# Kernel optimization log

Hardware: AMD Instinct MI355X
Metric: run time of the kernel (lower is better)

## Reference

```python
import jax, jax.numpy as jnp
import numpy as np

B, N, DIM = 4, 2048, 1024
HEADS, DIM_HEAD = 16, 64
INNER = HEADS * DIM_HEAD  # 1024
SCALE = DIM_HEAD ** -0.5

def setup_inputs() -> dict:
    key = jax.random.key(0)
    k1, k2, k3 = jax.random.split(key, 3)
    x = jax.random.normal(k1, (B, N, DIM), dtype=jnp.float32)
    w_qkv = jax.random.normal(k2, (DIM, 3 * INNER), dtype=jnp.float32) * (DIM ** -0.5)
    w_out = jax.random.normal(k3, (INNER, DIM), dtype=jnp.float32) * (INNER ** -0.5)
    b_out = jnp.zeros((DIM,), dtype=jnp.float32)
    return {"x": x, "w_qkv": w_qkv, "w_out": w_out, "b_out": b_out}

def reference(x, w_qkv, w_out, b_out):
    b, n, _ = x.shape
    qkv = x @ w_qkv  # [b, n, 3*inner]
    q, k, v = jnp.split(qkv, 3, axis=-1)
    # [b, n, h, d] -> [b, h, n, d]
    reshape = lambda t: t.reshape(b, n, HEADS, DIM_HEAD).transpose(0, 2, 1, 3)
    q, k, v = reshape(q), reshape(k), reshape(v)
    dots = jnp.einsum('bhqd,bhkd->bhqk', q, k) * SCALE
    attn = jax.nn.softmax(dots, axis=-1)
    out = jnp.einsum('bhqk,bhkd->bhqd', attn, v)
    out = out.transpose(0, 2, 1, 3).reshape(b, n, INNER)
    return out @ w_out + b_out
```

## Files before the change

### kernel.cpp

```cpp
#include <hip/hip_runtime.h>

typedef unsigned short u16;
typedef __bf16 bf16_t;
typedef bf16_t bf16x8 __attribute__((ext_vector_type(8)));
typedef float f32x4 __attribute__((ext_vector_type(4)));
typedef float f32x16 __attribute__((ext_vector_type(16)));
typedef u16 u16x8 __attribute__((ext_vector_type(8)));
typedef u16 u16x4 __attribute__((ext_vector_type(4)));
typedef unsigned uint2v __attribute__((ext_vector_type(2)));

#define B_     4
#define N_     2048
#define DIM_   1024
#define HEADS_ 16
#define DH_    64
#define INNER_ 1024
#define QKV3_  3072
#define SCALE_ 0.125f
#define LOG2E_ 1.44269504089f

__device__ __forceinline__ u16 f2bf(float f) {
  union { float f; unsigned u; } v; v.f = f;
  unsigned r = v.u + 0x7FFFu + ((v.u >> 16) & 1u);
  return (u16)(r >> 16);
}
__device__ __forceinline__ u16 bfbits(float f) {
  bf16_t b = (bf16_t)f;
  return __builtin_bit_cast(u16, b);
}
__device__ __forceinline__ unsigned packbf(float lo, float hi) {
  return (unsigned)bfbits(lo) | ((unsigned)bfbits(hi) << 16);
}

#if __has_builtin(__builtin_amdgcn_exp2f)
#define EXP2F(x) __builtin_amdgcn_exp2f(x)
#else
#define EXP2F(x) __expf((x) * 0.69314718056f)
#endif

typedef __attribute__((address_space(1))) const unsigned int ga_u32;
typedef __attribute__((address_space(3))) unsigned int ls_u32;
__device__ __forceinline__ void gload16(const void* g, void* l) {
  __builtin_amdgcn_global_load_lds((ga_u32*)g, (ls_u32*)l, 16, 0, 0);
}

__global__ __launch_bounds__(256) void cvt_f32_bf16(const float* __restrict__ in,
                                                    u16* __restrict__ out, int n8) {
  int i = blockIdx.x * 256 + threadIdx.x;
  if (i < n8) {
    const float4* p = (const float4*)(in + (size_t)i * 8);
    float4 a = p[0], b = p[1];
    u16x8 o;
    o[0] = f2bf(a.x); o[1] = f2bf(a.y); o[2] = f2bf(a.z); o[3] = f2bf(a.w);
    o[4] = f2bf(b.x); o[5] = f2bf(b.y); o[6] = f2bf(b.z); o[7] = f2bf(b.w);
    *(u16x8*)(out + (size_t)i * 8) = o;
  }
}

__global__ __launch_bounds__(256) void transp_w(const float* __restrict__ in,
                                                u16* __restrict__ out, int Kd, int Nd) {
  __shared__ float t[32][33];
  int n0 = blockIdx.x * 32, k0 = blockIdx.y * 32;
  int tx = threadIdx.x & 31, ty = threadIdx.x >> 5;
#pragma unroll
  for (int i = 0; i < 4; i++)
    t[ty + i * 8][tx] = in[(size_t)(k0 + ty + i * 8) * Nd + n0 + tx];
  __syncthreads();
#pragma unroll
  for (int i = 0; i < 4; i++)
    out[(size_t)(n0 + ty + i * 8) * Kd + k0 + tx] = f2bf(t[tx][ty + i * 8]);
}

__global__ __launch_bounds__(512, 2) void gemm_qkv(const u16* __restrict__ A,
                                                   const u16* __restrict__ BT,
                                                   u16* __restrict__ qbuf,
                                                   u16* __restrict__ ktiled,
                                                   u16* __restrict__ vtiled) {
  constexpr int K = DIM_;
  constexpr int KT = K / 64;
  __shared__ alignas(16) u16 ldsA[2][256 * 64];
  __shared__ alignas(16) u16 ldsB[2][256 * 64];
  const int tid = threadIdx.x;
  const int lane = tid & 63, wid = tid >> 6;
  const int l16 = lane & 15, lg = lane >> 4;
  const int wm = wid >> 2, wn = wid & 3;

  int bid = blockIdx.x;
  bid = (bid & 7) * 48 + (bid >> 3);
  const int tm = bid / 12, tn = bid % 12;
  const int m0 = tm << 8, n0 = tn << 8;

  const int srow_in = lane >> 3;
  const int soff = ((lane & 7) ^ srow_in) * 8;

  f32x4 acc[8][4];
#pragma unroll
  for (int i = 0; i < 8; i++)
#pragma unroll
    for (int j = 0; j < 4; j++) acc[i][j] = f32x4{0.f, 0.f, 0.f, 0.f};

#define STG_(kk, buf)                                                              \
  do {                                                                             \
    const int k1_ = (kk) << 6;                                                     \
    char* bA_ = (char*)&ldsA[(buf)][0];                                            \
    char* bB_ = (char*)&ldsB[(buf)][0];                                            \
    _Pragma("unroll")                                                              \
    for (int i_ = 0; i_ < 4; i_++) {                                               \
      const int rb_ = i_ * 64 + wid * 8;                                           \
      gload16(A  + (size_t)(m0 + rb_ + srow_in) * K + k1_ + soff, bA_ + rb_ * 128);\
      gload16(BT + (size_t)(n0 + rb_ + srow_in) * K + k1_ + soff, bB_ + rb_ * 128);\
    }                                                                              \
  } while (0)

  STG_(0, 0);

  for (int kt = 0; kt < KT; kt++) {
    asm volatile("s_waitcnt vmcnt(0)" ::: "memory");
    __builtin_amdgcn_s_barrier();
    if (kt + 1 < KT) STG_(kt + 1, (kt + 1) & 1);

    const char* cA = (const char*)&ldsA[kt & 1][0];
    const char* cB = (const char*)&ldsB[kt & 1][0];

    bf16x8 bf[4][2];
#pragma unroll
    for (int nf = 0; nf < 4; nf++) {
      const int row = wn * 64 + nf * 16 + l16;
      const int rb = row * 128, swz = (row & 7) << 4;
      bf[nf][0] = *(const bf16x8*)(cB + rb + ((lg * 16) ^ swz));
      bf[nf][1] = *(const bf16x8*)(cB + rb + ((64 + lg * 16) ^ swz));
    }
#pragma unroll
    for (int half = 0; half < 2; half++) {
      bf16x8 af[4][2];
#pragma unroll
      for (int m = 0; m < 4; m++) {
        const int row = wm * 128 + (half * 4 + m) * 16 + l16;
        const int rb = row * 128, swz = (row & 7) << 4;
        af[m][0] = *(const bf16x8*)(cA + rb + ((lg * 16) ^ swz));
        af[m][1] = *(const bf16x8*)(cA + rb + ((64 + lg * 16) ^ swz));
      }
      __builtin_amdgcn_s_setprio(1);
#pragma unroll
      for (int m = 0; m < 4; m++)
#pragma unroll
        for (int nf = 0; nf < 4; nf++) {
          f32x4 c = acc[half * 4 + m][nf];
          c = __builtin_amdgcn_mfma_f32_16x16x32_bf16(af[m][0], bf[nf][0], c, 0, 0, 0);
          c = __builtin_amdgcn_mfma_f32_16x16x32_bf16(af[m][1], bf[nf][1], c, 0, 0, 0);
          acc[half * 4 + m][nf] = c;
        }
      __builtin_amdgcn_s_setprio(0);
    }
  }
#undef STG_

  const int seg = n0 >> 10;
#pragma unroll
  for (int mf = 0; mf < 8; mf++) {
#pragma unroll
    for (int nf = 0; nf < 4; nf++) {
      const int row = m0 + wm * 128 + mf * 16 + lg * 4;
      const int col = n0 + wn * 64 + nf * 16 + l16;
      if (seg == 0) {
#pragma unroll
        for (int j = 0; j < 4; j++)
          qbuf[(size_t)(row + j) * INNER_ + col] = f2bf(acc[mf][nf][j]);
      } else if (seg == 1) {
        const int kd = col - 1024;
        const int h = kd >> 6, s = (kd >> 3) & 7, e = kd & 7;
#pragma unroll
        for (int j = 0; j < 4; j++) {
          const int rr = row + j;
          const int b = rr >> 11, n = rr & (N_ - 1);
          ktiled[(((size_t)(b * HEADS_ + h) * 32 + (n >> 6)) << 12) +
                 (s << 9) + ((n & 63) << 3) + e] = f2bf(acc[mf][nf][j]);
        }
      } else {
        const int vd = col - 2048;
        const int h = vd >> 6, d = vd & 63;
#pragma unroll
        for (int j = 0; j < 4; j++) {
          const int rr = row + j;
          const int b = rr >> 11, n = rr & (N_ - 1);
          vtiled[(((size_t)(b * HEADS_ + h) * 32 + (n >> 6)) << 12) +
                 (((n >> 3) & 7) << 9) + (d << 3) + (n & 7)] = f2bf(acc[mf][nf][j]);
        }
      }
    }
  }
}

__global__ __launch_bounds__(256) void gemm_bt(const u16* __restrict__ A,
                                               const u16* __restrict__ BT,
                                               float* __restrict__ Cp,
                                               const float* __restrict__ bias,
                                               int M, int N, int K) {
  __shared__ alignas(16) u16 ldsA[2][128 * 64];
  __shared__ alignas(16) u16 ldsB[2][128 * 64];
  const int tid = threadIdx.x;
  const int lane = tid & 63, wid = tid >> 6;
  const int l16 = lane & 15, lg = lane >> 4;

  int bid = blockIdx.x;
  const int cpx = gridDim.x >> 3;
  bid = (bid & 7) * cpx + (bid >> 3);

  const int ntiles = N >> 7;
  const int tm = bid / ntiles, tn = bid % ntiles;
  const int m0 = tm << 7, n0 = tn << 7;
  const int wr = wid >> 1, wc = wid & 1;

  const int srow_in = lane >> 3;
  const int soff = ((lane & 7) ^ srow_in) * 8;

  f32x4 acc[4][4];
#pragma unroll
  for (int i = 0; i < 4; i++)
#pragma unroll
    for (int j = 0; j < 4; j++) acc[i][j] = f32x4{0.f, 0.f, 0.f, 0.f};

  const int KSTEPS = K >> 6;

#define GSTAGE_(kk, buf)                                                           \
  do {                                                                             \
    const int k1_ = (kk) << 6;                                                     \
    char* bA_ = (char*)&ldsA[(buf)][0];                                            \
    char* bB_ = (char*)&ldsB[(buf)][0];                                            \
    _Pragma("unroll")                                                              \
    for (int i_ = 0; i_ < 4; i_++) {                                               \
      const int rb_ = wid * 32 + i_ * 8;                                           \
      gload16(A  + (size_t)(m0 + rb_ + srow_in) * K + k1_ + soff, bA_ + rb_ * 128);\
      gload16(BT + (size_t)(n0 + rb_ + srow_in) * K + k1_ + soff, bB_ + rb_ * 128);\
    }                                                                              \
  } while (0)

  GSTAGE_(0, 0);
  GSTAGE_(1, 1);

  for (int ks = 0; ks < KSTEPS; ks++) {
    if (ks + 1 < KSTEPS) asm volatile("s_waitcnt vmcnt(8)" ::: "memory");
    else                 asm volatile("s_waitcnt vmcnt(0)" ::: "memory");
    __builtin_amdgcn_s_barrier();

    const char* cA = (const char*)&ldsA[ks & 1][0];
    const char* cB = (const char*)&ldsB[ks & 1][0];

    bf16x8 bf[4][2];
#pragma unroll
    for (int n = 0; n < 4; n++) {
      int row = wc * 64 + n * 16 + l16;
      int rb = row * 128, swz = (row & 7) << 4;
      bf[n][0] = *(const bf16x8*)(cB + rb + ((lg * 16) ^ swz));
      bf[n][1] = *(const bf16x8*)(cB + rb + ((64 + lg * 16) ^ swz));
    }
    __builtin_amdgcn_s_setprio(1);
#pragma unroll
    for (int mm = 0; mm < 4; mm++) {
      int row = wr * 64 + mm * 16 + l16;
      int rb = row * 128, swz = (row & 7) << 4;
      bf16x8 af0 = *(const bf16x8*)(cA + rb + ((lg * 16) ^ swz));
      bf16x8 af1 = *(const bf16x8*)(cA + rb + ((64 + lg * 16) ^ swz));
#pragma unroll
      for (int n = 0; n < 4; n++) {
        acc[mm][n] = __builtin_amdgcn_mfma_f32_16x16x32_bf16(af0, bf[n][0], acc[mm][n], 0, 0, 0);
        acc[mm][n] = __builtin_amdgcn_mfma_f32_16x16x32_bf16(af1, bf[n][1], acc[mm][n], 0, 0, 0);
      }
    }
    __builtin_amdgcn_s_setprio(0);

    __builtin_amdgcn_s_barrier();
    if (ks + 2 < KSTEPS) GSTAGE_(ks + 2, ks & 1);
  }
#undef GSTAGE_

#pragma unroll
  for (int mm = 0; mm < 4; mm++) {
#pragma unroll
    for (int n = 0; n < 4; n++) {
      int row = m0 + wr * 64 + mm * 16 + lg * 4;
      int col = n0 + wc * 64 + n * 16 + l16;
#pragma unroll
      for (int j = 0; j < 4; j++)
        Cp[(size_t)(row + j) * N + col] = acc[mm][n][j] + bias[col];
    }
  }
}

__global__ __launch_bounds__(512, 4) void attn_fwd(const u16* __restrict__ qbuf,
                                                   const u16* __restrict__ ktiled,
                                                   const u16* __restrict__ vtiled,
                                                   u16* __restrict__ abuf) {
  __shared__ alignas(16) u16 ldsK[3][64 * 64];
  __shared__ alignas(16) u16 ldsV[3][64 * 64];

  const int tid = threadIdx.x;
  const int lane = tid & 63, wid = tid >> 6;
  const int l32 = lane & 31, hl = lane >> 5;

  int bid = blockIdx.x;
  bid = (bid & 7) * 64 + (bid >> 3);
  const int bh = bid >> 3, qt = bid & 7;
  const int b = bh >> 4, h = bh & 15;
  const int q0 = qt * 256 + wid * 32;

  constexpr float QS = SCALE_ * LOG2E_;
  bf16x8 qf[4];
  {
    const u16* qrow = qbuf + (size_t)(b * N_ + q0 + l32) * INNER_ + h * DH_ + hl * 8;
#pragma unroll
    for (int step = 0; step < 4; step++) {
      bf16x8 t = *(const bf16x8*)(qrow + step * 16);
#pragma unroll
      for (int i = 0; i < 8; i++) t[i] = (bf16_t)((float)t[i] * QS);
      qf[step] = t;
    }
  }

  const u16* kts = ktiled + (size_t)bh * 131072 + tid * 8;
  const u16* vts = vtiled + (size_t)bh * 131072 + tid * 8;
  const int sdst = wid << 10;

  const int kofs = (hl << 10) + (l32 << 4);

  float lrow = 0.f;
  f32x16 acc[2];
#pragma unroll
  for (int i = 0; i < 16; i++) { acc[0][i] = 0.f; acc[1][i] = 0.f; }

  gload16(kts, (char*)ldsK + sdst);
  gload16(vts, (char*)ldsV + sdst);
  gload16(kts + 4096, (char*)ldsK + 8192 + sdst);
  gload16(vts + 4096, (char*)ldsV + 8192 + sdst);

  const int NT = N_ / 64;
  int cur = 0, pre = 2;

  for (int kt = 0; kt < NT; ++kt) {
    if (kt < NT - 1) asm volatile("s_waitcnt vmcnt(2)" ::: "memory");
    else             asm volatile("s_waitcnt vmcnt(0)" ::: "memory");
    __builtin_amdgcn_s_barrier();
    if (kt + 2 < NT) {
      gload16(kts + (size_t)(kt + 2) * 4096, (char*)ldsK + pre * 8192 + sdst);
      gload16(vts + (size_t)(kt + 2) * 4096, (char*)ldsV + pre * 8192 + sdst);
    }

    const char* Kb = (const char*)ldsK + cur * 8192;
    const char* Vb = (const char*)ldsV + cur * 8192;

    f32x16 s[2];
    __builtin_amdgcn_s_setprio(1);
#pragma unroll
    for (int ktile = 0; ktile < 2; ktile++) {
      f32x16 c;
#pragma unroll
      for (int i = 0; i < 16; i++) c[i] = 0.f;
      const char* rb = Kb + (ktile << 9) + kofs;
#pragma unroll
      for (int step = 0; step < 4; step++) {
        bf16x8 kf = *(const bf16x8*)(rb + (step << 11));
        c = __builtin_amdgcn_mfma_f32_32x32x16_bf16(kf, qf[step], c, 0, 0, 0);
      }
      s[ktile] = c;
    }
    __builtin_amdgcn_s_setprio(0);

    float ps0 = 0.f, ps1 = 0.f;
#pragma unroll
    for (int ktile = 0; ktile < 2; ktile++)
#pragma unroll
      for (int i = 0; i < 16; i += 2) {
        const float p0 = EXP2F(s[ktile][i]);
        const float p1 = EXP2F(s[ktile][i + 1]);
        s[ktile][i] = p0; s[ktile][i + 1] = p1;
        ps0 += p0; ps1 += p1;
      }
    lrow += ps0 + ps1;

    bf16x8 pb[4];
#pragma unroll
    for (int ktile = 0; ktile < 2; ktile++)
#pragma unroll
      for (int par = 0; par < 2; par++) {
        const int rb8 = par * 8;
        const unsigned c0 = packbf(s[ktile][rb8 + 0], s[ktile][rb8 + 1]);
        const unsigned c1 = packbf(s[ktile][rb8 + 2], s[ktile][rb8 + 3]);
        const unsigned c2 = packbf(s[ktile][rb8 + 4], s[ktile][rb8 + 5]);
        const unsigned c3 = packbf(s[ktile][rb8 + 6], s[ktile][rb8 + 7]);
        const uint2v r02 = __builtin_amdgcn_permlane32_swap(c0, c2, false, false);
        const uint2v r13 = __builtin_amdgcn_permlane32_swap(c1, c3, false, false);
        union { unsigned u[4]; bf16x8 v; } w;
        w.u[0] = r02[0]; w.u[1] = r13[0]; w.u[2] = r02[1]; w.u[3] = r13[1];
        pb[ktile * 2 + par] = w.v;
      }

    __builtin_amdgcn_s_setprio(1);
#pragma unroll
    for (int dtile = 0; dtile < 2; dtile++) {
      const char* rb = Vb + (dtile << 9) + kofs;
      f32x16 c = acc[dtile];
#pragma unroll
      for (int step = 0; step < 4; step++) {
        bf16x8 vf = *(const bf16x8*)(rb + (step << 11));
        c = __builtin_amdgcn_mfma_f32_32x32x16_bf16(vf, pb[step], c, 0, 0, 0);
      }
      acc[dtile] = c;
    }
    __builtin_amdgcn_s_setprio(0);

    cur = (cur == 2) ? 0 : cur + 1;
    pre = (pre == 2) ? 0 : pre + 1;
  }

  lrow += __shfl_xor(lrow, 32);
  const float inv = 1.f / lrow;
  const size_t row = (size_t)(b * N_ + q0 + l32);
#pragma unroll
  for (int dtile = 0; dtile < 2; dtile++)
#pragma unroll
    for (int g = 0; g < 4; g++) {
      u16x4 w;
#pragma unroll
      for (int j = 0; j < 4; j++) w[j] = bfbits(acc[dtile][g * 4 + j] * inv);
      const int d = dtile * 32 + g * 8 + hl * 4;
      *(u16x4*)(abuf + row * INNER_ + h * DH_ + d) = w;
    }
}

extern "C" void kernel_launch(void* const* d_in, const int* in_sizes, int n_in,
                              void* d_out, int out_size, void* d_ws, size_t ws_size,
                              hipStream_t stream) {
  const float* x     = (const float*)d_in[0];
  const float* w_qkv = (const float*)d_in[1];
  const float* w_out = (const float*)d_in[2];
  const float* b_out = (const float*)d_in[3];
  float* out = (float*)d_out;

  char* ws = (char*)d_ws;
  u16* xb     = (u16*)(ws);
  u16* wqkvT  = (u16*)(ws + (size_t)(16 << 20));
  u16* woutT  = (u16*)(ws + (size_t)(22 << 20));
  u16* qbuf   = (u16*)(ws + (size_t)(24 << 20));
  u16* ktiled = (u16*)(ws + (size_t)(40 << 20));
  u16* vtiled = (u16*)(ws + (size_t)(56 << 20));
  u16* abuf   = xb;

  cvt_f32_bf16<<<4096, 256, 0, stream>>>(x, xb, (B_ * N_ * DIM_) / 8);
  transp_w<<<dim3(QKV3_ / 32, DIM_ / 32), 256, 0, stream>>>(w_qkv, wqkvT, DIM_, QKV3_);
  transp_w<<<dim3(DIM_ / 32, INNER_ / 32), 256, 0, stream>>>(w_out, woutT, INNER_, DIM_);
  gemm_qkv<<<384, 512, 0, stream>>>(xb, wqkvT, qbuf, ktiled, vtiled);
  attn_fwd<<<512, 512, 0, stream>>>(qbuf, ktiled, vtiled, abuf);
  gemm_bt<<<(B_ * N_ / 128) * (DIM_ / 128), 256, 0, stream>>>(
      abuf, woutT, out, b_out, B_ * N_, DIM_, INNER_);
}
```

Baseline: 193.8 us.

## Retile QKV GEMM to 256x384 tiles with triple-buffered K=32 pipeline

Changes the QKV projection GEMM from 256x256 tiles to 256x384, so it launches 256 blocks instead of 384, which on a 256-CU part should fill the device in a single wave. The K loop now steps by 32 with three LDS buffers and prefetches two stages ahead, waiting on a partial vmcnt so loads overlap compute. The LDS swizzle is adjusted for 64-byte rows, and the Q/K/V segment choice moves to per-fragment because a 384-wide tile can cross a segment boundary. More accumulators per thread (48 f32x4) raise register pressure, and the smaller K step means more barriers.

```diff
diff --git a/kernel.cpp b/kernel.cpp
--- a/kernel.cpp
+++ b/kernel.cpp
@@ -77,91 +77,83 @@
                                                    u16* __restrict__ ktiled,
                                                    u16* __restrict__ vtiled) {
   constexpr int K = DIM_;
-  constexpr int KT = K / 64;
-  __shared__ alignas(16) u16 ldsA[2][256 * 64];
-  __shared__ alignas(16) u16 ldsB[2][256 * 64];
+  constexpr int KS = K / 32;
+  __shared__ alignas(16) u16 ldsA[3][256 * 32];
+  __shared__ alignas(16) u16 ldsB[3][384 * 32];
   const int tid = threadIdx.x;
   const int lane = tid & 63, wid = tid >> 6;
   const int l16 = lane & 15, lg = lane >> 4;
   const int wm = wid >> 2, wn = wid & 3;
 
   int bid = blockIdx.x;
-  bid = (bid & 7) * 48 + (bid >> 3);
-  const int tm = bid / 12, tn = bid % 12;
-  const int m0 = tm << 8, n0 = tn << 8;
-
-  const int srow_in = lane >> 3;
-  const int soff = ((lane & 7) ^ srow_in) * 8;
-
-  f32x4 acc[8][4];
+  bid = (bid & 7) * 32 + (bid >> 3);
+  const int tm = bid >> 3, tn = bid & 7;
+  const int m0 = tm << 8, n0 = tn * 384;
+
+  const int srow = tid >> 2;
+  const int soff = ((tid & 3) ^ (srow & 3)) * 8;
+  const u16* Asrc = A  + (size_t)(m0 + srow) * K + soff;
+  const u16* Bsrc = BT + (size_t)(n0 + srow) * K + soff;
+  const int sdst = wid << 10;
+
+  f32x4 acc[8][6];
 #pragma unroll
   for (int i = 0; i < 8; i++)
 #pragma unroll
-    for (int j = 0; j < 4; j++) acc[i][j] = f32x4{0.f, 0.f, 0.f, 0.f};
-
-#define STG_(kk, buf)                                                              \
-  do {                                                                             \
-    const int k1_ = (kk) << 6;                                                     \
-    char* bA_ = (char*)&ldsA[(buf)][0];                                            \
-    char* bB_ = (char*)&ldsB[(buf)][0];                                            \
-    _Pragma("unroll")                                                              \
-    for (int i_ = 0; i_ < 4; i_++) {                                               \
-      const int rb_ = i_ * 64 + wid * 8;                                           \
-      gload16(A  + (size_t)(m0 + rb_ + srow_in) * K + k1_ + soff, bA_ + rb_ * 128);\
-      gload16(BT + (size_t)(n0 + rb_ + srow_in) * K + k1_ + soff, bB_ + rb_ * 128);\
-    }                                                                              \
+    for (int j = 0; j < 6; j++) acc[i][j] = f32x4{0.f, 0.f, 0.f, 0.f};
+
+#define STG_(kk, buf)                                                        \
+  do {                                                                       \
+    const int kb_ = (kk) << 5;                                               \
+    gload16(Asrc + kb_,                 (char*)&ldsA[(buf)][0] + sdst);      \
+    gload16(Asrc + (size_t)128 * K + kb_, (char*)&ldsA[(buf)][0] + 8192 + sdst); \
+    gload16(Bsrc + kb_,                 (char*)&ldsB[(buf)][0] + sdst);      \
+    gload16(Bsrc + (size_t)128 * K + kb_, (char*)&ldsB[(buf)][0] + 8192 + sdst); \
+    gload16(Bsrc + (size_t)256 * K + kb_, (char*)&ldsB[(buf)][0] + 16384 + sdst);\
   } while (0)
 
   STG_(0, 0);
-
-  for (int kt = 0; kt < KT; kt++) {
-    asm volatile("s_waitcnt vmcnt(0)" ::: "memory");
+  STG_(1, 1);
+
+  int cur = 0, pre = 2;
+  for (int ks = 0; ks < KS; ks++) {
+    if (ks < KS - 1) asm volatile("s_waitcnt vmcnt(5)" ::: "memory");
+    else             asm volatile("s_waitcnt vmcnt(0)" ::: "memory");
     __builtin_amdgcn_s_barrier();
-    if (kt + 1 < KT) STG_(kt + 1, (kt + 1) & 1);
-
-    const char* cA = (const char*)&ldsA[kt & 1][0];
-    const char* cB = (const char*)&ldsB[kt & 1][0];
-
-    bf16x8 bf[4][2];
-#pragma unroll
-    for (int nf = 0; nf < 4; nf++) {
-      const int row = wn * 64 + nf * 16 + l16;
-      const int rb = row * 128, swz = (row & 7) << 4;
-      bf[nf][0] = *(const bf16x8*)(cB + rb + ((lg * 16) ^ swz));
-      bf[nf][1] = *(const bf16x8*)(cB + rb + ((64 + lg * 16) ^ swz));
-    }
-#pragma unroll
-    for (int half = 0; half < 2; half++) {
-      bf16x8 af[4][2];
-#pragma unroll
-      for (int m = 0; m < 4; m++) {
-        const int row = wm * 128 + (half * 4 + m) * 16 + l16;
-        const int rb = row * 128, swz = (row & 7) << 4;
-        af[m][0] = *(const bf16x8*)(cA + rb + ((lg * 16) ^ swz));
-        af[m][1] = *(const bf16x8*)(cA + rb + ((64 + lg * 16) ^ swz));
-      }
-      __builtin_amdgcn_s_setprio(1);
-#pragma unroll
-      for (int m = 0; m < 4; m++)
-#pragma unroll
-        for (int nf = 0; nf < 4; nf++) {
-          f32x4 c = acc[half * 4 + m][nf];
-          c = __builtin_amdgcn_mfma_f32_16x16x32_bf16(af[m][0], bf[nf][0], c, 0, 0, 0);
-          c = __builtin_amdgcn_mfma_f32_16x16x32_bf16(af[m][1], bf[nf][1], c, 0, 0, 0);
-          acc[half * 4 + m][nf] = c;
-        }
-      __builtin_amdgcn_s_setprio(0);
-    }
+    if (ks + 2 < KS) STG_(ks + 2, pre);
+
+    const char* cA = (const char*)&ldsA[cur][0];
+    const char* cB = (const char*)&ldsB[cur][0];
+
+    bf16x8 bf[6];
+#pragma unroll
+    for (int nf = 0; nf < 6; nf++) {
+      const int row = wn * 96 + nf * 16 + l16;
+      bf[nf] = *(const bf16x8*)(cB + row * 64 + ((lg * 16) ^ ((row & 3) << 4)));
+    }
+    __builtin_amdgcn_s_setprio(1);
+#pragma unroll
+    for (int mf = 0; mf < 8; mf++) {
+      const int row = wm * 128 + mf * 16 + l16;
+      bf16x8 af = *(const bf16x8*)(cA + row * 64 + ((lg * 16) ^ ((row & 3) << 4)));
+#pragma unroll
+      for (int nf = 0; nf < 6; nf++)
+        acc[mf][nf] = __builtin_amdgcn_mfma_f32_16x16x32_bf16(af, bf[nf], acc[mf][nf], 0, 0, 0);
+    }
+    __builtin_amdgcn_s_setprio(0);
+
+    cur = (cur == 2) ? 0 : cur + 1;
+    pre = (pre == 2) ? 0 : pre + 1;
   }
 #undef STG_
 
-  const int seg = n0 >> 10;
 #pragma unroll
   for (int mf = 0; mf < 8; mf++) {
 #pragma unroll
-    for (int nf = 0; nf < 4; nf++) {
+    for (int nf = 0; nf < 6; nf++) {
       const int row = m0 + wm * 128 + mf * 16 + lg * 4;
-      const int col = n0 + wn * 64 + nf * 16 + l16;
+      const int col = n0 + wn * 96 + nf * 16 + l16;
+      const int seg = (n0 + wn * 96 + nf * 16) >> 10;
       if (seg == 0) {
 #pragma unroll
         for (int j = 0; j < 4; j++)
@@ -448,7 +440,7 @@
   cvt_f32_bf16<<<4096, 256, 0, stream>>>(x, xb, (B_ * N_ * DIM_) / 8);
   transp_w<<<dim3(QKV3_ / 32, DIM_ / 32), 256, 0, stream>>>(w_qkv, wqkvT, DIM_, QKV3_);
   transp_w<<<dim3(DIM_ / 32, INNER_ / 32), 256, 0, stream>>>(w_out, woutT, INNER_, DIM_);
-  gemm_qkv<<<384, 512, 0, stream>>>(xb, wqkvT, qbuf, ktiled, vtiled);
+  gemm_qkv<<<256, 512, 0, stream>>>(xb, wqkvT, qbuf, ktiled, vtiled);
   attn_fwd<<<512, 512, 0, stream>>>(qbuf, ktiled, vtiled, abuf);
   gemm_bt<<<(B_ * N_ / 128) * (DIM_ / 128), 256, 0, stream>>>(
       abuf, woutT, out, b_out, B_ * N_, DIM_, INNER_);
```

Measured after the change: 188.3 us. 1.03x faster.
